# Kernel optimization log

Hardware: AMD Instinct MI355X
Metric: run time of the kernel (lower is better)

Reference implementation:

```python
import jax, jax.numpy as jnp
import numpy as np

D_MODEL = 1024
NUM_HEADS = 16
D_HEAD = D_MODEL // NUM_HEADS
B, S = 2, 2048


def setup_inputs() -> dict:
    key = jax.random.key(0)
    ks = jax.random.split(key, 9)
    s = 1.0 / np.sqrt(D_MODEL)
    return {
        "query": jax.random.normal(ks[0], (B, S, D_MODEL), dtype=jnp.float32),
        "key": jax.random.normal(ks[1], (B, S, D_MODEL), dtype=jnp.float32),
        "value": jax.random.normal(ks[2], (B, S, D_MODEL), dtype=jnp.float32),
        "Wq": jax.random.normal(ks[3], (D_MODEL, D_MODEL), dtype=jnp.float32) * s,
        "bq": jnp.zeros((D_MODEL,), dtype=jnp.float32),
        "Wk": jax.random.normal(ks[4], (D_MODEL, D_MODEL), dtype=jnp.float32) * s,
        "bk": jnp.zeros((D_MODEL,), dtype=jnp.float32),
        "Wv": jax.random.normal(ks[5], (D_MODEL, D_MODEL), dtype=jnp.float32) * s,
        "bv": jnp.zeros((D_MODEL,), dtype=jnp.float32),
    }


def reference(query, key, value, Wq, bq, Wk, bk, Wv, bv):
    b, sq, d = query.shape
    sk = key.shape[1]
    h, dh = NUM_HEADS, D_HEAD
    # nn.Linear: x @ W^T + b, then split heads
    q = (query @ Wq.T + bq).reshape(b, sq, h, dh)
    k = (key @ Wk.T + bk).reshape(b, sk, h, dh)
    v = (value @ Wv.T + bv).reshape(b, sk, h, dh)
    # scaled dot-product attention: scores = QK^T / sqrt(d_head)
    scores = jnp.einsum("bqhd,bkhd->bhqk", q, k) / np.sqrt(dh).astype(np.float32)
    attn = jax.nn.softmax(scores, axis=-1)  # [b, h, sq, sk]
    ctx = jnp.einsum("bhqk,bkhd->bqhd", attn, v)
    context = ctx.reshape(b, sq, h * dh)
    # original returns attn flattened heads-major: (num_heads*batch, sq, sk)
    attn_out = jnp.transpose(attn, (1, 0, 2, 3)).reshape(h * b, sq, sk)
    return context, attn_out
```

## Files before the change

kernel.cpp:

```cpp
#include <hip/hip_runtime.h>


typedef __attribute__((ext_vector_type(8))) short bf16x8;
typedef __attribute__((ext_vector_type(4))) float f32x4;

#define MFMA16(a, b, c) __builtin_amdgcn_mfma_f32_16x16x32_bf16((a), (b), (c), 0, 0, 0)

static __device__ __forceinline__ unsigned short f2bf(float x) {
    __bf16 b = (__bf16)x;
    return __builtin_bit_cast(unsigned short, b);
}
static __device__ __forceinline__ float bf2f(unsigned short s) {
    return __builtin_bit_cast(float, ((unsigned int)s) << 16);
}

static __device__ __forceinline__ void gload16(const unsigned short* g, unsigned short* l) {
    __builtin_amdgcn_global_load_lds(
        (const __attribute__((address_space(1))) unsigned int*)g,
        (__attribute__((address_space(3))) unsigned int*)l, 16, 0, 0);
}

__global__ __launch_bounds__(256, 3) void qkv_proj(
    const float* __restrict__ query, const float* __restrict__ key_, const float* __restrict__ value,
    const float* __restrict__ Wq, const float* __restrict__ bq,
    const float* __restrict__ Wk, const float* __restrict__ bk,
    const float* __restrict__ Wv, const float* __restrict__ bv,
    unsigned short* __restrict__ qb_ws, unsigned short* __restrict__ kb_ws,
    unsigned short* __restrict__ vt_ws)
{
    __shared__ unsigned short sA[128 * 40];
    __shared__ unsigned short sB[128 * 40];

    const int z = blockIdx.z;
    const float* __restrict__ X    = (z == 0) ? query : (z == 1) ? key_ : value;
    const float* __restrict__ W    = (z == 0) ? Wq    : (z == 1) ? Wk   : Wv;
    const float* __restrict__ bias = (z == 0) ? bq    : (z == 1) ? bk   : bv;

    const int t = threadIdx.x;
    const int l = t & 63;
    const int w = t >> 6;
    const int lr = l & 15;
    const int lk = (l >> 4) * 8;
    const int m0 = blockIdx.y * 128;
    const int n0 = blockIdx.x * 128;
    const int wr = (w >> 1) * 64;
    const int wc = (w & 1) * 64;
    const int srow = t >> 1;
    const int sc0 = (t & 1) * 16;

    f32x4 acc[4][4];
#pragma unroll
    for (int i = 0; i < 4; i++)
#pragma unroll
        for (int j = 0; j < 4; j++) acc[i][j] = (f32x4){0.f, 0.f, 0.f, 0.f};

    float4 fa[4], fb[4];
#pragma unroll
    for (int u = 0; u < 4; u++) {
        fa[u] = *(const float4*)(&X[(size_t)(m0 + srow) * 1024 + sc0 + 4 * u]);
        fb[u] = *(const float4*)(&W[(size_t)(n0 + srow) * 1024 + sc0 + 4 * u]);
    }

    for (int kk = 0; kk < 1024; kk += 32) {
        __syncthreads();
#pragma unroll
        for (int u = 0; u < 4; u++) {
            ushort4 ah, bh;
            ah.x = f2bf(fa[u].x); ah.y = f2bf(fa[u].y);
            ah.z = f2bf(fa[u].z); ah.w = f2bf(fa[u].w);
            bh.x = f2bf(fb[u].x); bh.y = f2bf(fb[u].y);
            bh.z = f2bf(fb[u].z); bh.w = f2bf(fb[u].w);
            const int si = srow * 40 + sc0 + 4 * u;
            *(ushort4*)(&sA[si]) = ah;
            *(ushort4*)(&sB[si]) = bh;
        }
        __syncthreads();
        if (kk + 32 < 1024) {
#pragma unroll
            for (int u = 0; u < 4; u++) {
                fa[u] = *(const float4*)(&X[(size_t)(m0 + srow) * 1024 + kk + 32 + sc0 + 4 * u]);
                fb[u] = *(const float4*)(&W[(size_t)(n0 + srow) * 1024 + kk + 32 + sc0 + 4 * u]);
            }
        }
        bf16x8 Ah[4], Bh[4];
#pragma unroll
        for (int i = 0; i < 4; i++) {
            Ah[i] = *(const bf16x8*)(&sA[(wr + i * 16 + lr) * 40 + lk]);
            Bh[i] = *(const bf16x8*)(&sB[(wc + i * 16 + lr) * 40 + lk]);
        }
        __builtin_amdgcn_s_setprio(1);
#pragma unroll
        for (int i = 0; i < 4; i++)
#pragma unroll
            for (int j = 0; j < 4; j++)
                acc[i][j] = MFMA16(Ah[i], Bh[j], acc[i][j]);
        __builtin_amdgcn_s_setprio(0);
    }

#pragma unroll
    for (int i = 0; i < 4; i++)
#pragma unroll
        for (int j = 0; j < 4; j++) {
            const int gcol = n0 + wc + j * 16 + lr;
            const float bb = bias[gcol];
            const int grow0 = m0 + wr + i * 16 + (l >> 4) * 4;
            if (z == 2) {
                ushort4 pk;
                pk.x = f2bf(acc[i][j][0] + bb);
                pk.y = f2bf(acc[i][j][1] + bb);
                pk.z = f2bf(acc[i][j][2] + bb);
                pk.w = f2bf(acc[i][j][3] + bb);
                *(ushort4*)(&vt_ws[(size_t)gcol * 4096 + grow0]) = pk;
            } else if (z == 1) {
#pragma unroll
                for (int r = 0; r < 4; r++)
                    kb_ws[(size_t)(grow0 + r) * 1024 + gcol] = f2bf(acc[i][j][r] + bb);
            } else {
#pragma unroll
                for (int r = 0; r < 4; r++)
                    qb_ws[(size_t)(grow0 + r) * 1024 + gcol] =
                        f2bf((acc[i][j][r] + bb) * 0.1803368801111244f);
            }
        }
}

static __device__ __forceinline__ void stageK64(
    const unsigned short* __restrict__ kb_ws, unsigned short* dst,
    int b, int h, int k0, int w, int l)
{
    const int row = w * 8 + (l >> 3);
    const int col = ((l & 7) * 8) ^ ((row & 7) << 3);
    gload16(&kb_ws[(size_t)(b * 2048 + k0 + row) * 1024 + h * 64 + col], &dst[w * 512]);
}
static __device__ __forceinline__ void stageV64(
    const unsigned short* __restrict__ vt_ws, unsigned short* dst,
    int b, int h, int k0, int w, int l)
{
    const int d = w * 8 + (l >> 3);
    const int kk = ((l & 7) * 8) ^ ((d & 7) << 3);
    gload16(&vt_ws[(size_t)(h * 64 + d) * 4096 + b * 2048 + k0 + kk], &dst[w * 512]);
}
static __device__ __forceinline__ void stageWin256(
    const unsigned short* __restrict__ kb_ws, unsigned short* dst,
    int b, int h, int k0, int w, int l)
{
#pragma unroll
    for (int u = 0; u < 4; u++) {
        const int row = w * 32 + u * 8 + (l >> 3);
        const int col = ((l & 7) * 8) ^ ((row & 7) << 3);
        gload16(&kb_ws[(size_t)(b * 2048 + k0 + row) * 1024 + h * 64 + col],
                &dst[w * 2048 + u * 512]);
    }
}

static __device__ __forceinline__ void scores64(
    const unsigned short* sK, const bf16x8 (&qf)[2],
    int lr, int lg, f32x4 (&sc)[4])
{
#pragma unroll
    for (int n = 0; n < 4; n++) sc[n] = (f32x4){0.f, 0.f, 0.f, 0.f};
    __builtin_amdgcn_s_setprio(1);
#pragma unroll
    for (int n = 0; n < 4; n++) {
        const int row = n * 16 + lr;
#pragma unroll
        for (int kc = 0; kc < 2; kc++) {
            const int idx = (row * 64 + kc * 32 + lg * 8) ^ ((row & 7) << 3);
            const bf16x8 kf = *(const bf16x8*)(&sK[idx]);
            sc[n] = MFMA16(kf, qf[kc], sc[n]);
        }
    }
    __builtin_amdgcn_s_setprio(0);
}

#define SP_STRIDE 264

static __device__ __forceinline__ void doTileQKP(
    const unsigned short* sK, const unsigned short* sV, const bf16x8 (&qf)[2],
    char* sPb, f32x4 (&pv)[4], int half, int q0, int lr, int lg)
{
    f32x4 sc[4];
    scores64(sK, qf, lr, lg, sc);

    {
        char* const prow = sPb + (q0 + lr) * SP_STRIDE + half * 128;
#pragma unroll
        for (int n = 0; n < 4; n++) {
            float4 e;
            e.x = exp2f(sc[n][0]);
            e.y = exp2f(sc[n][1]);
            e.z = exp2f(sc[n][2]);
            e.w = exp2f(sc[n][3]);
            uint2 pk;
            pk.x = (unsigned int)f2bf(e.x) | ((unsigned int)f2bf(e.y) << 16);
            pk.y = (unsigned int)f2bf(e.z) | ((unsigned int)f2bf(e.w) << 16);
            *(uint2*)(prow + n * 32 + lg * 8) = pk;
        }
    }
    __builtin_amdgcn_s_setprio(1);
#pragma unroll
    for (int kcl = 0; kcl < 2; kcl++) {
        const bf16x8 pa = *(const bf16x8*)(sPb + (q0 + lr) * SP_STRIDE + half * 128 +
                                           kcl * 64 + lg * 16);
#pragma unroll
        for (int n = 0; n < 4; n++) {
            const int vrow = n * 16 + lr;
            const bf16x8 vb = *(const bf16x8*)(
                &sV[(vrow * 64 + kcl * 32 + lg * 8) ^ ((vrow & 7) << 3)]);
            pv[n] = MFMA16(pa, vb, pv[n]);
        }
    }
    __builtin_amdgcn_s_setprio(0);
}

__global__ __launch_bounds__(512, 4) void attn_fused(
    const unsigned short* __restrict__ qb_ws, const unsigned short* __restrict__ kb_ws,
    const unsigned short* __restrict__ vt_ws,
    float* __restrict__ ctx_out, float* __restrict__ attn_out)
{
    __shared__ unsigned short smem[33280];
    unsigned short* const kwin0 = smem;
    unsigned short* const kwin1 = smem + 16384;
    unsigned short* const sKA   = smem;
    unsigned short* const sKB   = smem + 4096;
    unsigned short* const sVA   = smem + 8192;
    unsigned short* const sVB   = smem + 12288;
    char* const sPb             = (char*)(smem + 16384);

    const int t = threadIdx.x;
    const int l = t & 63;
    const int w = t >> 6;
    const int lr = l & 15;
    const int lg = l >> 4;
    const int o  = (blockIdx.x & 7) * 64 + (blockIdx.x >> 3);
    const int qb = o & 15;
    const int h  = (o >> 4) & 15;
    const int b  = o >> 8;
    const int q0 = w * 16;

    bf16x8 qf[2];
    {
        const int grow = b * 2048 + qb * 128 + q0 + lr;
#pragma unroll
        for (int kc = 0; kc < 2; kc++)
            qf[kc] = *(const bf16x8*)(&qb_ws[(size_t)grow * 1024 + h * 64 + kc * 32 + lg * 8]);
    }

    float La = 0.f;

    stageWin256(kb_ws, kwin0, b, h, 0, w, l);
    __syncthreads();
    for (int kt = 0; kt < 8; kt++) {
        unsigned short* cur = (kt & 1) ? kwin1 : kwin0;
        unsigned short* nxt = (kt & 1) ? kwin0 : kwin1;
        if (kt < 7) stageWin256(kb_ws, nxt, b, h, (kt + 1) * 256, w, l);
#pragma unroll
        for (int sub = 0; sub < 4; sub++) {
            f32x4 sc[4];
            scores64(&cur[sub * 4096], qf, lr, lg, sc);
#pragma unroll
            for (int n = 0; n < 4; n++)
                La += (exp2f(sc[n][0]) + exp2f(sc[n][1])) +
                      (exp2f(sc[n][2]) + exp2f(sc[n][3]));
        }
        __syncthreads();
    }

    float invL;
    {
        float v = La;
        v += __shfl_xor(v, 16);
        v += __shfl_xor(v, 32);
        invL = 1.0f / v;
    }
    float il4[4];
#pragma unroll
    for (int i = 0; i < 4; i++) il4[i] = __shfl(invL, lg * 4 + i);
    float ilA[8];
#pragma unroll
    for (int i = 0; i < 8; i++) ilA[i] = __shfl(invL, 2 * i + (l >> 5));

    f32x4 pv[4];
#pragma unroll
    for (int n = 0; n < 4; n++) pv[n] = (f32x4){0.f, 0.f, 0.f, 0.f};

    const size_t abase = (size_t)(h * 2 + b) * 2048 + qb * 128;

    stageK64(kb_ws, sKA, b, h, 0, w, l);
    stageV64(vt_ws, sVA, b, h, 0, w, l);
    __syncthreads();
    for (int i = 0; i < 16; i++) {
        const int t0 = i * 2;
        stageK64(kb_ws, sKB, b, h, (t0 + 1) * 64, w, l);
        stageV64(vt_ws, sVB, b, h, (t0 + 1) * 64, w, l);
        doTileQKP(sKA, sVA, qf, sPb, pv, 0, q0, lr, lg);
        __syncthreads();
        if (i < 15) {
            stageK64(kb_ws, sKA, b, h, (t0 + 2) * 64, w, l);
            stageV64(vt_ws, sVA, b, h, (t0 + 2) * 64, w, l);
        }
        doTileQKP(sKB, sVB, qf, sPb, pv, 1, q0, lr, lg);
        {
            const int g0 = i * 128;
            const int rsel = l >> 5;
            const int lc = l & 31;
#pragma unroll
            for (int s = 0; s < 8; s++) {
                const int rq = q0 + 2 * s + rsel;
                ushort4 pk = *(const ushort4*)(sPb + rq * SP_STRIDE + lc * 8);
                const float il = ilA[s];
                f32x4 oo;
                oo[0] = bf2f(pk.x) * il;
                oo[1] = bf2f(pk.y) * il;
                oo[2] = bf2f(pk.z) * il;
                oo[3] = bf2f(pk.w) * il;
                __builtin_nontemporal_store(oo,
                    (f32x4*)(&attn_out[(abase + rq) * 2048 + g0 + lc * 4]));
            }
        }
        __syncthreads();
    }

#pragma unroll
    for (int r = 0; r < 4; r++) {
        const int qloc = q0 + lg * 4 + r;
        const int sq = qb * 128 + qloc;
        const float il = il4[r];
#pragma unroll
        for (int n = 0; n < 4; n++)
            __builtin_nontemporal_store(pv[n][r] * il,
                &ctx_out[((size_t)(b * 2048 + sq)) * 1024 + h * 64 + n * 16 + lr]);
    }
}

extern "C" void kernel_launch(void* const* d_in, const int* in_sizes, int n_in,
                              void* d_out, int out_size, void* d_ws, size_t ws_size,
                              hipStream_t stream)
{
    const float* query = (const float*)d_in[0];
    const float* key_  = (const float*)d_in[1];
    const float* value = (const float*)d_in[2];
    const float* Wq = (const float*)d_in[3];
    const float* bq = (const float*)d_in[4];
    const float* Wk = (const float*)d_in[5];
    const float* bk = (const float*)d_in[6];
    const float* Wv = (const float*)d_in[7];
    const float* bv = (const float*)d_in[8];

    unsigned short* qb_ws = (unsigned short*)d_ws;
    unsigned short* kb_ws = qb_ws + (size_t)4096 * 1024;
    unsigned short* vt_ws = kb_ws + (size_t)4096 * 1024;

    float* ctx_out  = (float*)d_out;
    float* attn_out = ctx_out + (size_t)2 * 2048 * 1024;

    dim3 g1(8, 32, 3);
    qkv_proj<<<g1, 256, 0, stream>>>(query, key_, value, Wq, bq, Wk, bk, Wv, bv,
                                     qb_ws, kb_ws, vt_ws);
    attn_fused<<<512, 512, 0, stream>>>(qb_ws, kb_ws, vt_ws, ctx_out, attn_out);
}
```

Before: 214.2 us.

## Transpose V projection through LDS and write attention probs in 1KB row groups

Result: slower. 244.1 us (+14.0%).

```diff
diff --git a/kernel.cpp b/kernel.cpp
--- a/kernel.cpp
+++ b/kernel.cpp
@@ -28,8 +28,10 @@
     unsigned short* __restrict__ qb_ws, unsigned short* __restrict__ kb_ws,
     unsigned short* __restrict__ vt_ws)
 {
-    __shared__ unsigned short sA[128 * 40];
-    __shared__ unsigned short sB[128 * 40];
+    __shared__ unsigned short smem1[16896];
+    unsigned short* const sA = smem1;
+    unsigned short* const sB = smem1 + 5120;
+    unsigned short* const sT = smem1;
 
     const int z = blockIdx.z;
     const float* __restrict__ X    = (z == 0) ? query : (z == 1) ? key_ : value;
@@ -97,31 +99,49 @@
         __builtin_amdgcn_s_setprio(0);
     }
 
-#pragma unroll
-    for (int i = 0; i < 4; i++)
-#pragma unroll
-        for (int j = 0; j < 4; j++) {
-            const int gcol = n0 + wc + j * 16 + lr;
-            const float bb = bias[gcol];
-            const int grow0 = m0 + wr + i * 16 + (l >> 4) * 4;
-            if (z == 2) {
+    if (z == 2) {
+        __syncthreads();
+#pragma unroll
+        for (int i = 0; i < 4; i++)
+#pragma unroll
+            for (int j = 0; j < 4; j++) {
+                const int gcol_l = wc + j * 16 + lr;
+                const float bb = bias[n0 + gcol_l];
                 ushort4 pk;
                 pk.x = f2bf(acc[i][j][0] + bb);
                 pk.y = f2bf(acc[i][j][1] + bb);
                 pk.z = f2bf(acc[i][j][2] + bb);
                 pk.w = f2bf(acc[i][j][3] + bb);
-                *(ushort4*)(&vt_ws[(size_t)gcol * 4096 + grow0]) = pk;
-            } else if (z == 1) {
-#pragma unroll
-                for (int r = 0; r < 4; r++)
-                    kb_ws[(size_t)(grow0 + r) * 1024 + gcol] = f2bf(acc[i][j][r] + bb);
-            } else {
-#pragma unroll
-                for (int r = 0; r < 4; r++)
-                    qb_ws[(size_t)(grow0 + r) * 1024 + gcol] =
-                        f2bf((acc[i][j][r] + bb) * 0.1803368801111244f);
+                *(ushort4*)(&sT[gcol_l * 132 + wr + i * 16 + (l >> 4) * 4]) = pk;
             }
-        }
+        __syncthreads();
+#pragma unroll
+        for (int s2 = 0; s2 < 16; s2++) {
+            const int rowl = s2 * 8 + (t >> 5);
+            const int coll = (t & 31) * 4;
+            *(ushort4*)(&vt_ws[(size_t)(n0 + rowl) * 4096 + m0 + coll]) =
+                *(const ushort4*)(&sT[rowl * 132 + coll]);
+        }
+    } else {
+#pragma unroll
+        for (int i = 0; i < 4; i++)
+#pragma unroll
+            for (int j = 0; j < 4; j++) {
+                const int gcol = n0 + wc + j * 16 + lr;
+                const float bb = bias[gcol];
+                const int grow0 = m0 + wr + i * 16 + (l >> 4) * 4;
+                if (z == 1) {
+#pragma unroll
+                    for (int r = 0; r < 4; r++)
+                        kb_ws[(size_t)(grow0 + r) * 1024 + gcol] = f2bf(acc[i][j][r] + bb);
+                } else {
+#pragma unroll
+                    for (int r = 0; r < 4; r++)
+                        qb_ws[(size_t)(grow0 + r) * 1024 + gcol] =
+                            f2bf((acc[i][j][r] + bb) * 0.1803368801111244f);
+                }
+            }
+    }
 }
 
 static __device__ __forceinline__ void stageK64(
@@ -173,17 +193,17 @@
     __builtin_amdgcn_s_setprio(0);
 }
 
-#define SP_STRIDE 264
+#define SP_STRIDE 520
 
 static __device__ __forceinline__ void doTileQKP(
     const unsigned short* sK, const unsigned short* sV, const bf16x8 (&qf)[2],
-    char* sPb, f32x4 (&pv)[4], int half, int q0, int lr, int lg)
+    char* sPb, f32x4 (&pv)[4], int halfB, int q0, int lr, int lg)
 {
     f32x4 sc[4];
     scores64(sK, qf, lr, lg, sc);
 
     {
-        char* const prow = sPb + (q0 + lr) * SP_STRIDE + half * 128;
+        char* const prow = sPb + (q0 + lr) * SP_STRIDE + halfB;
 #pragma unroll
         for (int n = 0; n < 4; n++) {
             float4 e;
@@ -200,7 +220,7 @@
     __builtin_amdgcn_s_setprio(1);
 #pragma unroll
     for (int kcl = 0; kcl < 2; kcl++) {
-        const bf16x8 pa = *(const bf16x8*)(sPb + (q0 + lr) * SP_STRIDE + half * 128 +
+        const bf16x8 pa = *(const bf16x8*)(sPb + (q0 + lr) * SP_STRIDE + halfB +
                                            kcl * 64 + lg * 16);
 #pragma unroll
         for (int n = 0; n < 4; n++) {
@@ -213,12 +233,32 @@
     __builtin_amdgcn_s_setprio(0);
 }
 
-__global__ __launch_bounds__(512, 4) void attn_fused(
+static __device__ __forceinline__ void storeGroup1KB(
+    const char* sPb, const float (&ilB)[16], float* __restrict__ attn_out,
+    size_t abase, int g, int q0, int l)
+{
+    const int g0 = g * 256;
+#pragma unroll
+    for (int s = 0; s < 16; s++) {
+        const int rq = q0 + s;
+        ushort4 pk = *(const ushort4*)(sPb + rq * SP_STRIDE + l * 8);
+        const float il = ilB[s];
+        f32x4 oo;
+        oo[0] = bf2f(pk.x) * il;
+        oo[1] = bf2f(pk.y) * il;
+        oo[2] = bf2f(pk.z) * il;
+        oo[3] = bf2f(pk.w) * il;
+        __builtin_nontemporal_store(oo,
+            (f32x4*)(&attn_out[(abase + rq) * 2048 + g0 + l * 4]));
+    }
+}
+
+__global__ __launch_bounds__(512, 2) void attn_fused(
     const unsigned short* __restrict__ qb_ws, const unsigned short* __restrict__ kb_ws,
     const unsigned short* __restrict__ vt_ws,
     float* __restrict__ ctx_out, float* __restrict__ attn_out)
 {
-    __shared__ unsigned short smem[33280];
+    __shared__ unsigned short smem[49664];
     unsigned short* const kwin0 = smem;
     unsigned short* const kwin1 = smem + 16384;
     unsigned short* const sKA   = smem;
@@ -276,9 +316,9 @@
     float il4[4];
 #pragma unroll
     for (int i = 0; i < 4; i++) il4[i] = __shfl(invL, lg * 4 + i);
-    float ilA[8];
-#pragma unroll
-    for (int i = 0; i < 8; i++) ilA[i] = __shfl(invL, 2 * i + (l >> 5));
+    float ilB[16];
+#pragma unroll
+    for (int i = 0; i < 16; i++) ilB[i] = __shfl(invL, i);
 
     f32x4 pv[4];
 #pragma unroll
@@ -289,35 +329,26 @@
     stageK64(kb_ws, sKA, b, h, 0, w, l);
     stageV64(vt_ws, sVA, b, h, 0, w, l);
     __syncthreads();
-    for (int i = 0; i < 16; i++) {
-        const int t0 = i * 2;
+    for (int g = 0; g < 8; g++) {
+        const int t0 = g * 4;
         stageK64(kb_ws, sKB, b, h, (t0 + 1) * 64, w, l);
         stageV64(vt_ws, sVB, b, h, (t0 + 1) * 64, w, l);
         doTileQKP(sKA, sVA, qf, sPb, pv, 0, q0, lr, lg);
         __syncthreads();
-        if (i < 15) {
-            stageK64(kb_ws, sKA, b, h, (t0 + 2) * 64, w, l);
-            stageV64(vt_ws, sVA, b, h, (t0 + 2) * 64, w, l);
-        }
-        doTileQKP(sKB, sVB, qf, sPb, pv, 1, q0, lr, lg);
-        {
-            const int g0 = i * 128;
-            const int rsel = l >> 5;
-            const int lc = l & 31;
-#pragma unroll
-            for (int s = 0; s < 8; s++) {
-                const int rq = q0 + 2 * s + rsel;
-                ushort4 pk = *(const ushort4*)(sPb + rq * SP_STRIDE + lc * 8);
-                const float il = ilA[s];
-                f32x4 oo;
-                oo[0] = bf2f(pk.x) * il;
-                oo[1] = bf2f(pk.y) * il;
-                oo[2] = bf2f(pk.z) * il;
-                oo[3] = bf2f(pk.w) * il;
-                __builtin_nontemporal_store(oo,
-                    (f32x4*)(&attn_out[(abase + rq) * 2048 + g0 + lc * 4]));
-            }
-        }
+        stageK64(kb_ws, sKA, b, h, (t0 + 2) * 64, w, l);
+        stageV64(vt_ws, sVA, b, h, (t0 + 2) * 64, w, l);
+        doTileQKP(sKB, sVB, qf, sPb, pv, 128, q0, lr, lg);
+        __syncthreads();
+        stageK64(kb_ws, sKB, b, h, (t0 + 3) * 64, w, l);
+        stageV64(vt_ws, sVB, b, h, (t0 + 3) * 64, w, l);
+        doTileQKP(sKA, sVA, qf, sPb, pv, 256, q0, lr, lg);
+        __syncthreads();
+        if (g < 7) {
+            stageK64(kb_ws, sKA, b, h, (t0 + 4) * 64, w, l);
+            stageV64(vt_ws, sVA, b, h, (t0 + 4) * 64, w, l);
+        }
+        doTileQKP(sKB, sVB, qf, sPb, pv, 384, q0, lr, lg);
+        storeGroup1KB(sPb, ilB, attn_out, abase, g, q0, l);
         __syncthreads();
     }
 
```
